# Performance work log

Measured on AMD Instinct MI355X. Metric: run time of the kernel, lower is better.

Reference implementation:

```python
import jax, jax.numpy as jnp
import numpy as np

LN_EPS = 1e-5  # nn.LayerNorm default
N_HEAD = 12


def layer_norm(x, w, b, eps=LN_EPS):
    m = jnp.mean(x, axis=-1, keepdims=True)
    v = jnp.var(x, axis=-1, keepdims=True)
    return (x - m) * jax.lax.rsqrt(v + eps) * w + b


def mha(x, in_proj_w, in_proj_b, out_w, out_b, n_head):
    # x: [B,S,D]; self-attention, q=k=v=x (torch nn.MultiheadAttention math)
    B, S, D = x.shape
    hd = D // n_head
    qkv = x @ in_proj_w.T + in_proj_b              # [B,S,3D]
    q, k, v = jnp.split(qkv, 3, axis=-1)
    q = q.reshape(B, S, n_head, hd)
    k = k.reshape(B, S, n_head, hd)
    v = v.reshape(B, S, n_head, hd)
    scale = 1.0 / jnp.sqrt(jnp.asarray(hd, x.dtype))
    scores = jnp.einsum('bqhd,bkhd->bhqk', q, k) * scale  # [B,H,S,S]
    attn = jax.nn.softmax(scores, axis=-1)
    o = jnp.einsum('bhqk,bkhd->bqhd', attn, v).reshape(B, S, D)
    return o @ out_w.T + out_b


def setup_inputs() -> dict:
    key = jax.random.key(0)
    ks = jax.random.split(key, 8)
    B, S, D = 4, 2048, 768
    d_ff = 4 * D
    sd = 0.02
    return {
        'x': jax.random.normal(ks[0], (B, S, D), jnp.float32),
        'ln1_w': jnp.ones((D,), jnp.float32),
        'ln1_b': jnp.zeros((D,), jnp.float32),
        'in_proj_w': jax.random.normal(ks[1], (3 * D, D), jnp.float32) * sd,
        'in_proj_b': jax.random.normal(ks[2], (3 * D,), jnp.float32) * sd,
        'out_w': jax.random.normal(ks[3], (D, D), jnp.float32) * sd,
        'out_b': jax.random.normal(ks[4], (D,), jnp.float32) * sd,
        'ln2_w': jnp.ones((D,), jnp.float32),
        'ln2_b': jnp.zeros((D,), jnp.float32),
        'fc_w': jax.random.normal(ks[5], (d_ff, D), jnp.float32) * sd,
        'fc_b': jnp.zeros((d_ff,), jnp.float32),
        'proj_w': jax.random.normal(ks[6], (D, d_ff), jnp.float32) * sd,
        'proj_b': jnp.zeros((D,), jnp.float32),
    }


def reference(x, ln1_w, ln1_b, in_proj_w, in_proj_b, out_w, out_b,
              ln2_w, ln2_b, fc_w, fc_b, proj_w, proj_b):
    h = layer_norm(x, ln1_w, ln1_b)
    x = x + mha(h, in_proj_w, in_proj_b, out_w, out_b, N_HEAD)
    h2 = layer_norm(x, ln2_w, ln2_b)
    mlp = jax.nn.gelu(h2 @ fc_w.T + fc_b, approximate=False) @ proj_w.T + proj_b
    return x + mlp
```

## Files before the change

kernel.cpp:

```cpp
#include <hip/hip_runtime.h>
#include <hip/hip_bf16.h>
#include <math.h>

#define D_MODEL 768
#define N_HEADS 12
#define HD 64
#define SEQ 2048
#define BATCH 4
#define M_ROWS 8192
#define D_FF 3072
#define QKV_DIM 2304
#define LN_EPS 1e-5f
#define Q_SCALE 0.18033688011112042f

typedef __attribute__((ext_vector_type(8))) short bf16x8;
typedef __attribute__((ext_vector_type(4))) float f32x4;
typedef __hip_bfloat16 bf16;

__device__ __forceinline__ void store_val(float* p, float v) { *p = v; }
__device__ __forceinline__ void store_val(bf16* p, float v) { *p = __float2bfloat16(v); }

__device__ __forceinline__ unsigned int bf16_bits(float v) {
    bf16 b = __float2bfloat16(v);
    unsigned short u;
    __builtin_memcpy(&u, &b, 2);
    return (unsigned int)u;
}

__device__ __forceinline__ void async_load16(const void* g, void* l) {
    __builtin_amdgcn_global_load_lds(
        (const __attribute__((address_space(1))) void*)g,
        (__attribute__((address_space(3))) void*)l, 16, 0, 0);
}

__global__ __launch_bounds__(256) void ln1_cast(
        const float* __restrict__ x, const float* __restrict__ w,
        const float* __restrict__ b, bf16* __restrict__ y,
        const float* __restrict__ s0, bf16* __restrict__ d0, int n0,
        const float* __restrict__ s1, bf16* __restrict__ d1, int n1,
        const float* __restrict__ s2, bf16* __restrict__ d2, int n2,
        const float* __restrict__ s3, bf16* __restrict__ d3, int n3) {
    int t = threadIdx.x;
    if (blockIdx.x >= M_ROWS) {
        int i = (blockIdx.x - M_ROWS) * 256 + t;
        const float* s; bf16* d; int local = i;
        if (local < n0) { s = s0; d = d0; }
        else {
            local -= n0;
            if (local < n1) { s = s1; d = d1; }
            else {
                local -= n1;
                if (local < n2) { s = s2; d = d2; }
                else {
                    local -= n2;
                    if (local >= n3) return;
                    s = s3; d = d3;
                }
            }
        }
        float4 v = ((const float4*)s)[local];
        d[local * 4 + 0] = __float2bfloat16(v.x);
        d[local * 4 + 1] = __float2bfloat16(v.y);
        d[local * 4 + 2] = __float2bfloat16(v.z);
        d[local * 4 + 3] = __float2bfloat16(v.w);
        return;
    }
    int row = blockIdx.x;
    const float* xr = x + (size_t)row * D_MODEL;
    bf16* yr = y + (size_t)row * D_MODEL;
    float v0 = xr[t], v1 = xr[t + 256], v2 = xr[t + 512];
    float s  = v0 + v1 + v2;
    float sq = v0 * v0 + v1 * v1 + v2 * v2;
    #pragma unroll
    for (int off = 32; off; off >>= 1) {
        s  += __shfl_xor(s, off);
        sq += __shfl_xor(sq, off);
    }
    __shared__ float ss[4], ssq[4];
    int wave = t >> 6;
    if ((t & 63) == 0) { ss[wave] = s; ssq[wave] = sq; }
    __syncthreads();
    s  = ss[0] + ss[1] + ss[2] + ss[3];
    sq = ssq[0] + ssq[1] + ssq[2] + ssq[3];
    float mean = s * (1.0f / D_MODEL);
    float var  = sq * (1.0f / D_MODEL) - mean * mean;
    float rstd = rsqrtf(var + LN_EPS);
    yr[t]       = __float2bfloat16((v0 - mean) * rstd * w[t]       + b[t]);
    yr[t + 256] = __float2bfloat16((v1 - mean) * rstd * w[t + 256] + b[t + 256]);
    yr[t + 512] = __float2bfloat16((v2 - mean) * rstd * w[t + 512] + b[t + 512]);
}

template <typename OutT>
__global__ __launch_bounds__(256) void ln_kernel(const float* __restrict__ x,
                                                 const float* __restrict__ w,
                                                 const float* __restrict__ b,
                                                 OutT* __restrict__ y) {
    int row = blockIdx.x;
    const float* xr = x + (size_t)row * D_MODEL;
    OutT* yr = y + (size_t)row * D_MODEL;
    int t = threadIdx.x;
    float v0 = xr[t], v1 = xr[t + 256], v2 = xr[t + 512];
    float s  = v0 + v1 + v2;
    float sq = v0 * v0 + v1 * v1 + v2 * v2;
    #pragma unroll
    for (int off = 32; off; off >>= 1) {
        s  += __shfl_xor(s, off);
        sq += __shfl_xor(sq, off);
    }
    __shared__ float ss[4], ssq[4];
    int wave = t >> 6;
    if ((t & 63) == 0) { ss[wave] = s; ssq[wave] = sq; }
    __syncthreads();
    s  = ss[0] + ss[1] + ss[2] + ss[3];
    sq = ssq[0] + ssq[1] + ssq[2] + ssq[3];
    float mean = s * (1.0f / D_MODEL);
    float var  = sq * (1.0f / D_MODEL) - mean * mean;
    float rstd = rsqrtf(var + LN_EPS);
    store_val(yr + t,       (v0 - mean) * rstd * w[t]       + b[t]);
    store_val(yr + t + 256, (v1 - mean) * rstd * w[t + 256] + b[t + 256]);
    store_val(yr + t + 512, (v2 - mean) * rstd * w[t + 512] + b[t + 512]);
}

__device__ __forceinline__ float gelu_exact(float v) {
    return 0.5f * v * (1.0f + erff(v * 0.70710678118654752f));
}

template <int FUSE, int BNT, typename OutT>
__global__ __launch_bounds__(256) void gemm_mfma(const bf16* __restrict__ A,
                                                 const bf16* __restrict__ W,
                                                 const float* __restrict__ bias,
                                                 const float* __restrict__ resid,
                                                 bf16* __restrict__ vt,
                                                 OutT* __restrict__ C,
                                                 int M, int N, int K) {
    const int BM = 128, BK = 32;
    const int MI = (BNT == 128) ? 4 : 2;
    const int BCH = BNT * 4 / 256;
    __shared__ __align__(16) bf16 As[BM * BK];
    __shared__ __align__(16) bf16 Bs[BNT * BK];
    int t = threadIdx.x;
    int wave = t >> 6, lane = t & 63;
    int m_base = blockIdx.y * BM, n_base = blockIdx.x * BNT;
    int wm = (BNT == 128) ? (wave >> 1) * 64 : wave * 32;
    int wn = (BNT == 128) ? (wave & 1) * 64 : 0;

    f32x4 acc[MI][4] = {};

    const bf16* Ag[2]; const bf16* Bg[2];
    bf16* Al[2]; bf16* Bl[2];
    #pragma unroll
    for (int r = 0; r < 2; r++) {
        int c = r * 256 + t;
        int row = c >> 2, ko = (c & 3) * 8;
        Ag[r] = A + (size_t)(m_base + row) * K + ko;
        Al[r] = As + (r * 256 + wave * 64) * 8;
        if (r < BCH) {
            Bg[r] = W + (size_t)(n_base + row) * K + ko;
            Bl[r] = Bs + (r * 256 + wave * 64) * 8;
        }
    }

    int fr = lane & 15;
    int fk = (lane >> 4) * 8;

    for (int k0 = 0; k0 < K; k0 += BK) {
        __syncthreads();
        #pragma unroll
        for (int r = 0; r < 2; r++) {
            async_load16(Ag[r] + k0, Al[r]);
            if (r < BCH) async_load16(Bg[r] + k0, Bl[r]);
        }
        __syncthreads();

        bf16x8 af[MI], bfr[4];
        #pragma unroll
        for (int mi = 0; mi < MI; mi++)
            af[mi] = *(const bf16x8*)&As[(wm + mi * 16 + fr) * BK + fk];
        #pragma unroll
        for (int ni = 0; ni < 4; ni++)
            bfr[ni] = *(const bf16x8*)&Bs[(wn + ni * 16 + fr) * BK + fk];
        #pragma unroll
        for (int mi = 0; mi < MI; mi++)
            #pragma unroll
            for (int ni = 0; ni < 4; ni++)
                acc[mi][ni] = __builtin_amdgcn_mfma_f32_16x16x32_bf16(
                    af[mi], bfr[ni], acc[mi][ni], 0, 0, 0);
    }

    int rq = (lane >> 4) * 4;
    int c_ = lane & 15;

    if (FUSE == 3 && n_base >= 1536) {
        bf16* T = As;
        int bb = m_base >> 11, s_off = m_base & 2047;
        int d0 = n_base - 1536;
        #pragma unroll
        for (int p = 0; p < 4; p++) {
            __syncthreads();
            if ((wave & 1) == (p >> 1)) {
                int ni0 = (p & 1) * 2;
                #pragma unroll
                for (int q = 0; q < 2; q++) {
                    int nd = ni0 + q;
                    float bv = bias[n_base + wn + nd * 16 + c_];
                    #pragma unroll
                    for (int mi = 0; mi < MI; mi++) {
                        unsigned int lo = bf16_bits(acc[mi][nd][0] + bv) |
                                          (bf16_bits(acc[mi][nd][1] + bv) << 16);
                        unsigned int hi = bf16_bits(acc[mi][nd][2] + bv) |
                                          (bf16_bits(acc[mi][nd][3] + bv) << 16);
                        uint2 pk; pk.x = lo; pk.y = hi;
                        int drel = q * 16 + c_;
                        int s = wm + mi * 16 + rq;
                        *(uint2*)&T[drel * 128 + s] = pk;
                    }
                }
            }
            __syncthreads();
            {
                int r = t >> 3, part = t & 7;
                int d = d0 + p * 32 + r;
                int hh = d >> 6, dd = d & 63;
                bf16* dstp = vt + ((size_t)(bb * N_HEADS + hh) * HD + dd) * SEQ + s_off + part * 16;
                uint4 v0 = *(const uint4*)&T[r * 128 + part * 16];
                uint4 v1 = *(const uint4*)&T[r * 128 + part * 16 + 8];
                *(uint4*)dstp = v0;
                *(uint4*)(dstp + 8) = v1;
            }
        }
        return;
    }

    float scale = (FUSE == 3 && n_base < 768) ? Q_SCALE : 1.0f;
    #pragma unroll
    for (int mi = 0; mi < MI; mi++) {
        #pragma unroll
        for (int ni = 0; ni < 4; ni++) {
            int col = n_base + wn + ni * 16 + c_;
            float bv = bias[col];
            #pragma unroll
            for (int reg = 0; reg < 4; reg++) {
                int row = m_base + wm + mi * 16 + rq + reg;
                float v = acc[mi][ni][reg] + bv;
                if (FUSE == 1) v = gelu_exact(v);
                if (FUSE == 2) v += resid[(size_t)row * N + col];
                if (FUSE == 3) v *= scale;
                store_val(C + (size_t)row * N + col, v);
            }
        }
    }
}

__global__ __launch_bounds__(256) void attn_mfma(const bf16* __restrict__ qkvb,
                                                 const bf16* __restrict__ vt,
                                                 bf16* __restrict__ o) {
    __shared__ __align__(16) bf16 Qs[2 * 128 * 32];
    __shared__ __align__(16) bf16 Ks[2 * 64 * 32];
    __shared__ __align__(16) bf16 Vts[2 * 64 * 32];
    __shared__ __align__(16) bf16 Ps[128 * 72];

    int t = threadIdx.x;
    int wave = t >> 6, lane = t & 63;
    int qt = blockIdx.x, h = blockIdx.y, b = blockIdx.z;
    int s0 = qt * 128;
    int wq = wave * 32;
    int c = lane & 15, rr = lane >> 4;

    const bf16* qbase  = qkvb + (size_t)b * SEQ * QKV_DIM + h * HD;
    const bf16* kbase  = qbase + D_MODEL;
    const bf16* vtbase = vt + (size_t)((b * N_HEADS + h) * HD) * SEQ;

    #pragma unroll
    for (int r = 0; r < 4; r++) {
        int lin = r * 256 + t;
        int kk = lin >> 9, qq = (lin >> 2) & 127, qo = lin & 3;
        async_load16(qbase + (size_t)(s0 + qq) * QKV_DIM + kk * 32 + qo * 8,
                     Qs + (size_t)(r * 256 + wave * 64) * 8);
    }
    __syncthreads();

    bf16x8 bq[2][2];
    #pragma unroll
    for (int m = 0; m < 2; m++)
        #pragma unroll
        for (int kk = 0; kk < 2; kk++)
            bq[m][kk] = *(const bf16x8*)&Qs[kk * 4096 + (wq + m * 16 + c) * 32 + rr * 8];

    f32x4 Oa[2][4] = {};
    float l_part[2] = {};

    for (int jt = 0; jt < SEQ; jt += 64) {
        __syncthreads();
        #pragma unroll
        for (int r = 0; r < 2; r++) {
            int lin = r * 256 + t;
            int kk = lin >> 8, jj = (lin >> 2) & 63, qo = lin & 3;
            async_load16(kbase + (size_t)(jt + jj) * QKV_DIM + kk * 32 + qo * 8,
                         Ks + (size_t)(r * 256 + wave * 64) * 8);
            async_load16(vtbase + (size_t)jj * SEQ + jt + kk * 32 + qo * 8,
                         Vts + (size_t)(r * 256 + wave * 64) * 8);
        }
        __syncthreads();

        f32x4 St[4][2] = {};
        #pragma unroll
        for (int kk = 0; kk < 2; kk++) {
            bf16x8 ak[4];
            #pragma unroll
            for (int jj = 0; jj < 4; jj++)
                ak[jj] = *(const bf16x8*)&Ks[kk * 2048 + (jj * 16 + c) * 32 + rr * 8];
            #pragma unroll
            for (int jj = 0; jj < 4; jj++)
                #pragma unroll
                for (int m = 0; m < 2; m++)
                    St[jj][m] = __builtin_amdgcn_mfma_f32_16x16x32_bf16(
                        ak[jj], bq[m][kk], St[jj][m], 0, 0, 0);
        }

        #pragma unroll
        for (int jj = 0; jj < 4; jj++) {
            #pragma unroll
            for (int m = 0; m < 2; m++) {
                float p0 = __builtin_amdgcn_exp2f(St[jj][m][0]);
                float p1 = __builtin_amdgcn_exp2f(St[jj][m][1]);
                float p2 = __builtin_amdgcn_exp2f(St[jj][m][2]);
                float p3 = __builtin_amdgcn_exp2f(St[jj][m][3]);
                l_part[m] += (p0 + p1) + (p2 + p3);
                uint2 pk;
                pk.x = bf16_bits(p0) | (bf16_bits(p1) << 16);
                pk.y = bf16_bits(p2) | (bf16_bits(p3) << 16);
                *(uint2*)&Ps[(wq + m * 16 + c) * 72 + jj * 16 + rr * 4] = pk;
            }
        }

        #pragma unroll
        for (int kk = 0; kk < 2; kk++) {
            bf16x8 ap[2];
            #pragma unroll
            for (int m = 0; m < 2; m++)
                ap[m] = *(const bf16x8*)&Ps[(wq + m * 16 + c) * 72 + kk * 32 + rr * 8];
            #pragma unroll
            for (int n = 0; n < 4; n++) {
                bf16x8 bv = *(const bf16x8*)&Vts[kk * 2048 + (n * 16 + c) * 32 + rr * 8];
                #pragma unroll
                for (int m = 0; m < 2; m++)
                    Oa[m][n] = __builtin_amdgcn_mfma_f32_16x16x32_bf16(
                        ap[m], bv, Oa[m][n], 0, 0, 0);
            }
        }
    }

    float lred[2];
    #pragma unroll
    for (int m = 0; m < 2; m++) {
        float l = l_part[m];
        l += __shfl_xor(l, 16);
        l += __shfl_xor(l, 32);
        lred[m] = l;
    }
    #pragma unroll
    for (int m = 0; m < 2; m++)
        #pragma unroll
        for (int rg = 0; rg < 4; rg++) {
            float inv = 1.0f / __shfl(lred[m], rr * 4 + rg);
            int q = s0 + wq + m * 16 + rr * 4 + rg;
            bf16* op = o + (size_t)(b * SEQ + q) * D_MODEL + h * HD;
            #pragma unroll
            for (int n = 0; n < 4; n++)
                op[n * 16 + c] = __float2bfloat16(Oa[m][n][rg] * inv);
        }
}

extern "C" void kernel_launch(void* const* d_in, const int* in_sizes, int n_in,
                              void* d_out, int out_size, void* d_ws, size_t ws_size,
                              hipStream_t stream) {
    const float* x         = (const float*)d_in[0];
    const float* ln1_w     = (const float*)d_in[1];
    const float* ln1_b     = (const float*)d_in[2];
    const float* in_proj_w = (const float*)d_in[3];
    const float* in_proj_b = (const float*)d_in[4];
    const float* out_w     = (const float*)d_in[5];
    const float* out_b     = (const float*)d_in[6];
    const float* ln2_w     = (const float*)d_in[7];
    const float* ln2_b     = (const float*)d_in[8];
    const float* fc_w      = (const float*)d_in[9];
    const float* fc_b      = (const float*)d_in[10];
    const float* proj_w    = (const float*)d_in[11];
    const float* proj_b    = (const float*)d_in[12];

    float* out = (float*)d_out;
    char*  ws  = (char*)d_ws;

    bf16* qkvb = (bf16*)ws;
    bf16* vt   = (bf16*)(ws + 37748736);
    bf16* ff   = (bf16*)ws;
    bf16* h    = (bf16*)(ws + 50331648);
    bf16* o    = (bf16*)(ws + 62914560);
    bf16* wbf  = (bf16*)(ws + 75497472);
    bf16* wqkv_b  = wbf;
    bf16* wout_b  = wqkv_b + (size_t)QKV_DIM * D_MODEL;
    bf16* wfc_b   = wout_b + (size_t)D_MODEL * D_MODEL;
    bf16* wproj_b = wfc_b  + (size_t)D_FF * D_MODEL;

    int n0 = QKV_DIM * D_MODEL / 4, n1 = D_MODEL * D_MODEL / 4;
    int n2 = D_FF * D_MODEL / 4,    n3 = D_MODEL * D_FF / 4;
    int cast_blocks = (n0 + n1 + n2 + n3 + 255) / 256;

    ln1_cast<<<M_ROWS + cast_blocks, 256, 0, stream>>>(
        x, ln1_w, ln1_b, h,
        in_proj_w, wqkv_b, n0, out_w, wout_b, n1, fc_w, wfc_b, n2, proj_w, wproj_b, n3);
    gemm_mfma<3, 128, bf16><<<dim3(QKV_DIM / 128, M_ROWS / 128), 256, 0, stream>>>(
        h, wqkv_b, in_proj_b, nullptr, vt, qkvb, M_ROWS, QKV_DIM, D_MODEL);
    attn_mfma<<<dim3(SEQ / 128, N_HEADS, BATCH), 256, 0, stream>>>(qkvb, vt, o);
    gemm_mfma<2, 64, float><<<dim3(D_MODEL / 64, M_ROWS / 128), 256, 0, stream>>>(
        o, wout_b, out_b, x, nullptr, out, M_ROWS, D_MODEL, D_MODEL);
    ln_kernel<bf16><<<M_ROWS, 256, 0, stream>>>(out, ln2_w, ln2_b, h);
    gemm_mfma<1, 128, bf16><<<dim3(D_FF / 128, M_ROWS / 128), 256, 0, stream>>>(
        h, wfc_b, fc_b, nullptr, nullptr, ff, M_ROWS, D_FF, D_MODEL);
    gemm_mfma<2, 64, float><<<dim3(D_MODEL / 64, M_ROWS / 128), 256, 0, stream>>>(
        ff, wproj_b, proj_b, out, nullptr, out, M_ROWS, D_MODEL, D_FF);
}
```

Measured before the change: 441.0 us.

## Rework GEMM with BK=64 swizzled LDS, swapped MFMA operands, vectorized epilogue

The GEMM kernel now uses a 64-wide K tile with an XOR-swizzled LDS layout to avoid bank conflicts. It swaps the MFMA operand order so each lane holds four consecutive output columns, which allows float4 bias and residual loads and vector stores. The N=768 GEMMs move from 64-wide to 128-wide tiles, which halves their block count. The V transpose that was fused into the QKV GEMM epilogue becomes a separate kernel, adding one launch and an extra read of V from global memory.

```diff
diff --git a/kernel.cpp b/kernel.cpp
--- a/kernel.cpp
+++ b/kernel.cpp
@@ -125,130 +125,129 @@
     return 0.5f * v * (1.0f + erff(v * 0.70710678118654752f));
 }
 
-template <int FUSE, int BNT, typename OutT>
+template <int FUSE, typename OutT>
 __global__ __launch_bounds__(256) void gemm_mfma(const bf16* __restrict__ A,
                                                  const bf16* __restrict__ W,
                                                  const float* __restrict__ bias,
                                                  const float* __restrict__ resid,
-                                                 bf16* __restrict__ vt,
                                                  OutT* __restrict__ C,
                                                  int M, int N, int K) {
-    const int BM = 128, BK = 32;
-    const int MI = (BNT == 128) ? 4 : 2;
-    const int BCH = BNT * 4 / 256;
-    __shared__ __align__(16) bf16 As[BM * BK];
-    __shared__ __align__(16) bf16 Bs[BNT * BK];
+    const int BK = 64;
+    __shared__ __align__(16) bf16 As[128 * BK];
+    __shared__ __align__(16) bf16 Bs[128 * BK];
     int t = threadIdx.x;
     int wave = t >> 6, lane = t & 63;
-    int m_base = blockIdx.y * BM, n_base = blockIdx.x * BNT;
-    int wm = (BNT == 128) ? (wave >> 1) * 64 : wave * 32;
-    int wn = (BNT == 128) ? (wave & 1) * 64 : 0;
-
-    f32x4 acc[MI][4] = {};
-
-    const bf16* Ag[2]; const bf16* Bg[2];
-    bf16* Al[2]; bf16* Bl[2];
-    #pragma unroll
-    for (int r = 0; r < 2; r++) {
-        int c = r * 256 + t;
-        int row = c >> 2, ko = (c & 3) * 8;
-        Ag[r] = A + (size_t)(m_base + row) * K + ko;
+    int m_base = blockIdx.y * 128, n_base = blockIdx.x * 128;
+    int wm = (wave >> 1) * 64, wn = (wave & 1) * 64;
+    int c = lane & 15, rr = lane >> 4;
+
+    f32x4 acc[4][4] = {};
+
+    const bf16* Ag[4]; const bf16* Bg[4];
+    bf16* Al[4]; bf16* Bl[4];
+    #pragma unroll
+    for (int r = 0; r < 4; r++) {
+        int s = r * 256 + t;
+        int row = s >> 3, p = s & 7;
+        int kc = p ^ (row & 7);
+        Ag[r] = A + (size_t)(m_base + row) * K + kc * 8;
+        Bg[r] = W + (size_t)(n_base + row) * K + kc * 8;
         Al[r] = As + (r * 256 + wave * 64) * 8;
-        if (r < BCH) {
-            Bg[r] = W + (size_t)(n_base + row) * K + ko;
-            Bl[r] = Bs + (r * 256 + wave * 64) * 8;
-        }
-    }
-
-    int fr = lane & 15;
-    int fk = (lane >> 4) * 8;
+        Bl[r] = Bs + (r * 256 + wave * 64) * 8;
+    }
 
     for (int k0 = 0; k0 < K; k0 += BK) {
         __syncthreads();
         #pragma unroll
-        for (int r = 0; r < 2; r++) {
+        for (int r = 0; r < 4; r++) {
             async_load16(Ag[r] + k0, Al[r]);
-            if (r < BCH) async_load16(Bg[r] + k0, Bl[r]);
+            async_load16(Bg[r] + k0, Bl[r]);
         }
         __syncthreads();
 
-        bf16x8 af[MI], bfr[4];
-        #pragma unroll
-        for (int mi = 0; mi < MI; mi++)
-            af[mi] = *(const bf16x8*)&As[(wm + mi * 16 + fr) * BK + fk];
-        #pragma unroll
-        for (int ni = 0; ni < 4; ni++)
-            bfr[ni] = *(const bf16x8*)&Bs[(wn + ni * 16 + fr) * BK + fk];
-        #pragma unroll
-        for (int mi = 0; mi < MI; mi++)
+        #pragma unroll
+        for (int kk = 0; kk < 2; kk++) {
+            int sw = ((kk * 4 + rr) ^ (c & 7)) * 8;
+            bf16x8 af[4], bfr[4];
+            #pragma unroll
+            for (int mi = 0; mi < 4; mi++)
+                af[mi] = *(const bf16x8*)&As[(wm + mi * 16 + c) * BK + sw];
             #pragma unroll
             for (int ni = 0; ni < 4; ni++)
-                acc[mi][ni] = __builtin_amdgcn_mfma_f32_16x16x32_bf16(
-                    af[mi], bfr[ni], acc[mi][ni], 0, 0, 0);
-    }
-
-    int rq = (lane >> 4) * 4;
-    int c_ = lane & 15;
-
-    if (FUSE == 3 && n_base >= 1536) {
-        bf16* T = As;
-        int bb = m_base >> 11, s_off = m_base & 2047;
-        int d0 = n_base - 1536;
-        #pragma unroll
-        for (int p = 0; p < 4; p++) {
-            __syncthreads();
-            if ((wave & 1) == (p >> 1)) {
-                int ni0 = (p & 1) * 2;
+                bfr[ni] = *(const bf16x8*)&Bs[(wn + ni * 16 + c) * BK + sw];
+            #pragma unroll
+            for (int mi = 0; mi < 4; mi++)
                 #pragma unroll
-                for (int q = 0; q < 2; q++) {
-                    int nd = ni0 + q;
-                    float bv = bias[n_base + wn + nd * 16 + c_];
-                    #pragma unroll
-                    for (int mi = 0; mi < MI; mi++) {
-                        unsigned int lo = bf16_bits(acc[mi][nd][0] + bv) |
-                                          (bf16_bits(acc[mi][nd][1] + bv) << 16);
-                        unsigned int hi = bf16_bits(acc[mi][nd][2] + bv) |
-                                          (bf16_bits(acc[mi][nd][3] + bv) << 16);
-                        uint2 pk; pk.x = lo; pk.y = hi;
-                        int drel = q * 16 + c_;
-                        int s = wm + mi * 16 + rq;
-                        *(uint2*)&T[drel * 128 + s] = pk;
-                    }
-                }
-            }
-            __syncthreads();
-            {
-                int r = t >> 3, part = t & 7;
-                int d = d0 + p * 32 + r;
-                int hh = d >> 6, dd = d & 63;
-                bf16* dstp = vt + ((size_t)(bb * N_HEADS + hh) * HD + dd) * SEQ + s_off + part * 16;
-                uint4 v0 = *(const uint4*)&T[r * 128 + part * 16];
-                uint4 v1 = *(const uint4*)&T[r * 128 + part * 16 + 8];
-                *(uint4*)dstp = v0;
-                *(uint4*)(dstp + 8) = v1;
-            }
-        }
-        return;
-    }
-
-    float scale = (FUSE == 3 && n_base < 768) ? Q_SCALE : 1.0f;
-    #pragma unroll
-    for (int mi = 0; mi < MI; mi++) {
+                for (int ni = 0; ni < 4; ni++)
+                    acc[mi][ni] = __builtin_amdgcn_mfma_f32_16x16x32_bf16(
+                        bfr[ni], af[mi], acc[mi][ni], 0, 0, 0);
+        }
+    }
+
+    #pragma unroll
+    for (int mi = 0; mi < 4; mi++) {
+        int m = m_base + wm + mi * 16 + c;
         #pragma unroll
         for (int ni = 0; ni < 4; ni++) {
-            int col = n_base + wn + ni * 16 + c_;
-            float bv = bias[col];
-            #pragma unroll
-            for (int reg = 0; reg < 4; reg++) {
-                int row = m_base + wm + mi * 16 + rq + reg;
-                float v = acc[mi][ni][reg] + bv;
-                if (FUSE == 1) v = gelu_exact(v);
-                if (FUSE == 2) v += resid[(size_t)row * N + col];
-                if (FUSE == 3) v *= scale;
-                store_val(C + (size_t)row * N + col, v);
-            }
-        }
-    }
+            int n0 = n_base + wn + ni * 16 + rr * 4;
+            float4 bv = *(const float4*)&bias[n0];
+            float v0 = acc[mi][ni][0] + bv.x;
+            float v1 = acc[mi][ni][1] + bv.y;
+            float v2 = acc[mi][ni][2] + bv.z;
+            float v3 = acc[mi][ni][3] + bv.w;
+            if (FUSE == 1) {
+                v0 = gelu_exact(v0); v1 = gelu_exact(v1);
+                v2 = gelu_exact(v2); v3 = gelu_exact(v3);
+            }
+            if (FUSE == 2) {
+                float4 rv = *(const float4*)&resid[(size_t)m * N + n0];
+                v0 += rv.x; v1 += rv.y; v2 += rv.z; v3 += rv.w;
+            }
+            if (FUSE == 3 && n0 < 768) {
+                v0 *= Q_SCALE; v1 *= Q_SCALE; v2 *= Q_SCALE; v3 *= Q_SCALE;
+            }
+            OutT* dst = C + (size_t)m * N + n0;
+            if (sizeof(OutT) == 4) {
+                float4 st = {v0, v1, v2, v3};
+                *(float4*)dst = st;
+            } else {
+                uint2 pk;
+                pk.x = bf16_bits(v0) | (bf16_bits(v1) << 16);
+                pk.y = bf16_bits(v2) | (bf16_bits(v3) << 16);
+                *(uint2*)dst = pk;
+            }
+        }
+    }
+}
+
+__global__ __launch_bounds__(256) void vtrans(const bf16* __restrict__ qkvb,
+                                              bf16* __restrict__ vt) {
+    __shared__ bf16 T[64 * 72];
+    int t = threadIdx.x;
+    int s0 = blockIdx.x * 64, h = blockIdx.y, b = blockIdx.z;
+    const bf16* src = qkvb + (size_t)(b * SEQ) * QKV_DIM + 2 * D_MODEL + h * HD;
+    #pragma unroll
+    for (int i = 0; i < 2; i++) {
+        int idx = i * 256 + t;
+        int sr = idx >> 3, ch = idx & 7;
+        uint4 v = *(const uint4*)(src + (size_t)(s0 + sr) * QKV_DIM + ch * 8);
+        *(uint4*)&T[sr * 72 + ch * 8] = v;
+    }
+    __syncthreads();
+    int dr = t >> 2, part = t & 3;
+    unsigned int w[8];
+    #pragma unroll
+    for (int i = 0; i < 8; i++) {
+        unsigned short a, bsh;
+        __builtin_memcpy(&a,   &T[(part * 16 + 2 * i    ) * 72 + dr], 2);
+        __builtin_memcpy(&bsh, &T[(part * 16 + 2 * i + 1) * 72 + dr], 2);
+        w[i] = (unsigned int)a | ((unsigned int)bsh << 16);
+    }
+    bf16* dst = vt + ((size_t)((b * N_HEADS + h) * HD + dr)) * SEQ + s0 + part * 16;
+    uint4 p0; p0.x = w[0]; p0.y = w[1]; p0.z = w[2]; p0.w = w[3];
+    uint4 p1; p1.x = w[4]; p1.y = w[5]; p1.z = w[6]; p1.w = w[7];
+    *(uint4*)dst = p0;
+    *(uint4*)(dst + 8) = p1;
 }
 
 __global__ __launch_bounds__(256) void attn_mfma(const bf16* __restrict__ qkvb,
@@ -409,14 +408,15 @@
     ln1_cast<<<M_ROWS + cast_blocks, 256, 0, stream>>>(
         x, ln1_w, ln1_b, h,
         in_proj_w, wqkv_b, n0, out_w, wout_b, n1, fc_w, wfc_b, n2, proj_w, wproj_b, n3);
-    gemm_mfma<3, 128, bf16><<<dim3(QKV_DIM / 128, M_ROWS / 128), 256, 0, stream>>>(
-        h, wqkv_b, in_proj_b, nullptr, vt, qkvb, M_ROWS, QKV_DIM, D_MODEL);
+    gemm_mfma<3, bf16><<<dim3(QKV_DIM / 128, M_ROWS / 128), 256, 0, stream>>>(
+        h, wqkv_b, in_proj_b, nullptr, qkvb, M_ROWS, QKV_DIM, D_MODEL);
+    vtrans<<<dim3(SEQ / 64, N_HEADS, BATCH), 256, 0, stream>>>(qkvb, vt);
     attn_mfma<<<dim3(SEQ / 128, N_HEADS, BATCH), 256, 0, stream>>>(qkvb, vt, o);
-    gemm_mfma<2, 64, float><<<dim3(D_MODEL / 64, M_ROWS / 128), 256, 0, stream>>>(
-        o, wout_b, out_b, x, nullptr, out, M_ROWS, D_MODEL, D_MODEL);
+    gemm_mfma<2, float><<<dim3(D_MODEL / 128, M_ROWS / 128), 256, 0, stream>>>(
+        o, wout_b, out_b, x, out, M_ROWS, D_MODEL, D_MODEL);
     ln_kernel<bf16><<<M_ROWS, 256, 0, stream>>>(out, ln2_w, ln2_b, h);
-    gemm_mfma<1, 128, bf16><<<dim3(D_FF / 128, M_ROWS / 128), 256, 0, stream>>>(
-        h, wfc_b, fc_b, nullptr, nullptr, ff, M_ROWS, D_FF, D_MODEL);
-    gemm_mfma<2, 64, float><<<dim3(D_MODEL / 64, M_ROWS / 128), 256, 0, stream>>>(
-        ff, wproj_b, proj_b, out, nullptr, out, M_ROWS, D_MODEL, D_FF);
-}
+    gemm_mfma<1, bf16><<<dim3(D_FF / 128, M_ROWS / 128), 256, 0, stream>>>(
+        h, wfc_b, fc_b, nullptr, ff, M_ROWS, D_FF, D_MODEL);
+    gemm_mfma<2, float><<<dim3(D_MODEL / 128, M_ROWS / 128), 256, 0, stream>>>(
+        ff, wproj_b, proj_b, out, out, M_ROWS, D_MODEL, D_FF);
+}
```

Measured after the change: 421.0 us. 1.05x faster.
